# Kernel optimization log

Measured on AMD Instinct MI355X. Metric: run time of the kernel, lower is better.

Reference implementation:

```python
import jax, jax.numpy as jnp
import numpy as np

B, T, S, E, H, D = 4, 1024, 1024, 1024, 16, 64


def _ln(x, g, b, eps=1e-5):
    m = x.mean(-1, keepdims=True)
    v = ((x - m) ** 2).mean(-1, keepdims=True)
    return (x - m) * jax.lax.rsqrt(v + eps) * g + b


def _mha(xq, xkv, mask4, Wq, Wk, Wv, Wo, bo):
    # Wq/Wk/Wv: [H, E, D] (stacked per-head bias-free linears)
    q = jnp.einsum('bte,hed->bhtd', xq, Wq)
    k = jnp.einsum('bse,hed->bhsd', xkv, Wk)
    v = jnp.einsum('bse,hed->bhsd', xkv, Wv)
    # NOTE: original scales by C**-0.5 with C = n_embd, not head_size
    wei = jnp.einsum('bhtd,bhsd->bhts', q, k) * (float(E) ** -0.5)
    wei = jnp.where(mask4 == 0, jnp.float32(-1e9), wei)
    wei = jax.nn.softmax(wei, axis=-1)
    o = jnp.einsum('bhts,bhsd->bhtd', wei, v)  # [B,H,T,D]
    b_, h_, t_, d_ = o.shape
    o = o.transpose(0, 2, 1, 3).reshape(b_, t_, h_ * d_)
    return o @ Wo + bo


def setup_inputs() -> dict:
    key = jax.random.key(0)
    ks = jax.random.split(key, 24)
    sd = 0.02
    inp = {
        'x': jax.random.normal(ks[0], (B, T, E), jnp.float32),
        'x_m': jnp.ones((B, 1, T), jnp.int32),
        'ca': jax.random.normal(ks[1], (B, S, E), jnp.float32),
        'ca_m': jnp.ones((B, 1, S), jnp.int32),
        'Wq_s': jax.random.normal(ks[2], (H, E, D), jnp.float32) * sd,
        'Wk_s': jax.random.normal(ks[3], (H, E, D), jnp.float32) * sd,
        'Wv_s': jax.random.normal(ks[4], (H, E, D), jnp.float32) * sd,
        'Wo_s': jax.random.normal(ks[5], (E, E), jnp.float32) * sd,
        'bo_s': jnp.zeros((E,), jnp.float32),
        'Wq_c': jax.random.normal(ks[6], (H, E, D), jnp.float32) * sd,
        'Wk_c': jax.random.normal(ks[7], (H, E, D), jnp.float32) * sd,
        'Wv_c': jax.random.normal(ks[8], (H, E, D), jnp.float32) * sd,
        'Wo_c': jax.random.normal(ks[9], (E, E), jnp.float32) * sd,
        'bo_c': jnp.zeros((E,), jnp.float32),
        'ln1_g': jnp.ones((E,), jnp.float32), 'ln1_b': jnp.zeros((E,), jnp.float32),
        'ln2_g': jnp.ones((E,), jnp.float32), 'ln2_b': jnp.zeros((E,), jnp.float32),
        'ln3_g': jnp.ones((E,), jnp.float32), 'ln3_b': jnp.zeros((E,), jnp.float32),
        'W1': jax.random.normal(ks[10], (E, 4 * E), jnp.float32) * sd,
        'b1': jnp.zeros((4 * E,), jnp.float32),
        'W2': jax.random.normal(ks[11], (4 * E, E), jnp.float32) * sd,
        'b2': jnp.zeros((E,), jnp.float32),
    }
    return inp


def reference(x, x_m, ca, ca_m, Wq_s, Wk_s, Wv_s, Wo_s, bo_s,
              Wq_c, Wk_c, Wv_c, Wo_c, bo_c,
              ln1_g, ln1_b, ln2_g, ln2_b, ln3_g, ln3_b,
              W1, b1, W2, b2):
    tril = jnp.tril(jnp.ones((T, T), jnp.int32))
    # self-attn mask: x_m [B,1,T] & tril [T,T] -> [B,1,T,T] (broadcast over heads)
    self_mask = x_m[:, :, None, :] * tril          # [B,1,T,T]
    cross_mask = ca_m[:, :, None, :]               # [B,1,1,S]
    x = x + _mha(_ln(x, ln1_g, ln1_b), _ln(x, ln1_g, ln1_b) if False else _ln(x, ln1_g, ln1_b), self_mask, Wq_s, Wk_s, Wv_s, Wo_s, bo_s)
    x = x + _mha(_ln(x, ln2_g, ln2_b), ca, cross_mask, Wq_c, Wk_c, Wv_c, Wo_c, bo_c)
    h = _ln(x, ln3_g, ln3_b)
    x = x + (jax.nn.relu(h @ W1 + b1) @ W2 + b2)
    return x
```

## Files before the change

### kernel.cpp

```cpp
#include <hip/hip_runtime.h>
#include <hip/hip_bf16.h>
#include <cstdint>
#include <cstddef>

typedef __attribute__((ext_vector_type(8))) short  s8v;
typedef __attribute__((ext_vector_type(4))) short  s4v;
typedef __attribute__((ext_vector_type(8))) __bf16 b8v;
typedef __attribute__((ext_vector_type(4))) float  f32x4;
typedef __attribute__((ext_vector_type(4))) unsigned u32x4;

__device__ __forceinline__ short f2bf(float f){
  unsigned u = __builtin_bit_cast(unsigned, f);
  unsigned r = (u + 0x7fffu + ((u >> 16) & 1u)) >> 16;
  return (short)(unsigned short)r;
}

__device__ __forceinline__ f32x4 mfma16(s8v a, s8v b, f32x4 c){
  return __builtin_amdgcn_mfma_f32_16x16x32_bf16(
      __builtin_bit_cast(b8v, a), __builtin_bit_cast(b8v, b), c, 0, 0, 0);
}

__device__ __forceinline__ unsigned cvtpk(float a, float b){
  unsigned w;
  asm("v_cvt_pk_bf16_f32 %0, %1, %2" : "=v"(w) : "v"(a), "v"(b));
  return w;
}

__global__ __launch_bounds__(256)
void ln_k(const float* __restrict__ x, const float* __restrict__ g,
          const float* __restrict__ b, short* __restrict__ out)
{
  const int row = blockIdx.x, tid = threadIdx.x;
  const float4 v = ((const float4*)(x + (size_t)row*1024))[tid];
  float s  = v.x+v.y+v.z+v.w;
  float s2 = v.x*v.x+v.y*v.y+v.z*v.z+v.w*v.w;
  #pragma unroll
  for (int off=32; off; off>>=1){ s += __shfl_down(s, off); s2 += __shfl_down(s2, off); }
  __shared__ float red[8];
  const int wave = tid>>6, lane = tid&63;
  if (lane==0){ red[wave]=s; red[4+wave]=s2; }
  __syncthreads();
  s  = red[0]+red[1]+red[2]+red[3];
  s2 = red[4]+red[5]+red[6]+red[7];
  const float mean = s*(1.f/1024.f);
  const float rstd = rsqrtf(s2*(1.f/1024.f) - mean*mean + 1e-5f);
  const float4 gv = ((const float4*)g)[tid];
  const float4 bv = ((const float4*)b)[tid];
  s4v o;
  o[0] = f2bf((v.x-mean)*rstd*gv.x + bv.x);
  o[1] = f2bf((v.y-mean)*rstd*gv.y + bv.y);
  o[2] = f2bf((v.z-mean)*rstd*gv.z + bv.z);
  o[3] = f2bf((v.w-mean)*rstd*gv.w + bv.w);
  *(s4v*)(out + (size_t)row*1024 + tid*4) = o;
}

__global__ __launch_bounds__(256)
void cast_k(const float* __restrict__ in, short* __restrict__ out)
{
  const int i = blockIdx.x*256 + threadIdx.x;
  const float4 v = ((const float4*)in)[i];
  s4v o; o[0]=f2bf(v.x); o[1]=f2bf(v.y); o[2]=f2bf(v.z); o[3]=f2bf(v.w);
  ((s4v*)out)[i] = o;
}

__global__ __launch_bounds__(256)
void tcast_k(const float* __restrict__ in, short* __restrict__ out, int E2, int D2)
{
  __shared__ float t[32][33];
  const int h  = blockIdx.z;
  const int e0 = blockIdx.x*32, d0 = blockIdx.y*32;
  const int tx = threadIdx.x & 31, ty = threadIdx.x >> 5;
  const float* ip = in + (size_t)h*E2*D2;
  #pragma unroll
  for (int r = ty; r < 32; r += 8)
    t[r][tx] = ip[(size_t)(e0+r)*D2 + d0 + tx];
  __syncthreads();
  short* op = out + (size_t)h*D2*E2;
  #pragma unroll
  for (int r = ty; r < 32; r += 8)
    op[(size_t)(d0+r)*E2 + e0 + tx] = f2bf(t[tx][r]);
}

__global__ __launch_bounds__(256)
void vtrans_k(const short* __restrict__ V, int ldv, short* __restrict__ Vt, int S, int H)
{
  __shared__ short t[32][34];
  const int bh = blockIdx.z;
  const int b = bh / H, h = bh % H;
  const int s0 = blockIdx.x*32, d0 = blockIdx.y*32;
  const int tx = threadIdx.x & 31, ty = threadIdx.x >> 5;
  const short* ip = V + (size_t)b*S*ldv + h*64;
  #pragma unroll
  for (int r = ty; r < 32; r += 8)
    t[r][tx] = ip[(size_t)(s0+r)*ldv + d0 + tx];
  __syncthreads();
  short* op = Vt + ((size_t)bh*64 + d0)*S + s0;
  #pragma unroll
  for (int r = ty; r < 32; r += 8)
    op[(size_t)r*S + tx] = t[tx][r];
}

__global__ __launch_bounds__(256)
void red2_k(const float* __restrict__ pa, const float* __restrict__ pb,
            const float* __restrict__ bias, const float* __restrict__ resid,
            float* __restrict__ out, int N)
{
  const int i = blockIdx.x*256 + threadIdx.x;
  const float4 va = ((const float4*)pa)[i];
  const float4 vb = ((const float4*)pb)[i];
  const float4 vr = ((const float4*)resid)[i];
  const float4 bv = ((const float4*)bias)[i & (N/4 - 1)];
  float4 o;
  o.x = va.x+vb.x+bv.x+vr.x; o.y = va.y+vb.y+bv.y+vr.y;
  o.z = va.z+vb.z+bv.z+vr.z; o.w = va.w+vb.w+bv.w+vr.w;
  ((float4*)out)[i] = o;
}

template<int BN, int BIAS, int RELU, int RESID, int WF32>
__global__ __launch_bounds__(256, 2)
void gemm_bt(const short* __restrict__ A, const short* __restrict__ Bt,
             const float* __restrict__ bias, const float* __restrict__ resid,
             short* __restrict__ Cb, float* __restrict__ Cf,
             int M, int N, int K)
{
  __shared__ short lds[3][128*32 + BN*32];
  const int nwg = gridDim.x * gridDim.y;
  int id = blockIdx.y * gridDim.x + blockIdx.x;
  id = (id & 7) * (nwg >> 3) + (id >> 3);
  const int bx = id % gridDim.x, by = id / gridDim.x;
  const int m0 = by*128, n0 = bx*BN;

  const int tid  = threadIdx.x;
  const int wave = tid>>6, lane = tid&63;
  const int lo = lane&15, hi = lane>>4;
  const int wm = wave>>1, wn = wave&1;

  constexpr int NJ = BN/32;
  constexpr int BC = BN>>6;
  f32x4 acc[4][NJ] = {};
  const int NK = K >> 5;

  auto stage = [&](int buf, int kt){
    const short* Ag = A  + (size_t)m0*K + kt*32;
    const short* Bg = Bt + (size_t)n0*K + kt*32;
    #pragma unroll
    for (int c=0;c<2;c++){
      const int q = (wave*2+c)*64 + lane;
      const int r = q>>2, cc = q&3;
      __builtin_amdgcn_global_load_lds(
        (const __attribute__((address_space(1))) void*)(Ag + (size_t)r*K + cc*8),
        (__attribute__((address_space(3))) void*)(&lds[buf][(wave*2+c)*512]),
        16, 0, 0);
    }
    #pragma unroll
    for (int c=0;c<BC;c++){
      const int q = (wave*BC+c)*64 + lane;
      const int r = q>>2, cc = q&3;
      __builtin_amdgcn_global_load_lds(
        (const __attribute__((address_space(1))) void*)(Bg + (size_t)r*K + cc*8),
        (__attribute__((address_space(3))) void*)(&lds[buf][4096 + (wave*BC+c)*512]),
        16, 0, 0);
    }
  };

  stage(0, 0);
  if (NK > 1) stage(1, 1);

  for (int kt=0; kt<NK; kt++){
    if (kt+1 < NK){
      if constexpr (BN==128) asm volatile("s_waitcnt vmcnt(4)" ::: "memory");
      else                   asm volatile("s_waitcnt vmcnt(3)" ::: "memory");
    } else {
      asm volatile("s_waitcnt vmcnt(0)" ::: "memory");
    }
    __builtin_amdgcn_s_barrier();
    __builtin_amdgcn_sched_barrier(0);
    if (kt+2 < NK) stage((kt+2)%3, kt+2);

    const short* la = &lds[kt%3][0];
    const short* lb = &lds[kt%3][4096];
    s8v af[4], bfr[NJ];
    #pragma unroll
    for (int i=0;i<4;i++)
      af[i] = *(const s8v*)(la + (wm*64 + i*16 + lo)*32 + hi*8);
    #pragma unroll
    for (int j=0;j<NJ;j++)
      bfr[j] = *(const s8v*)(lb + (wn*(BN/2) + j*16 + lo)*32 + hi*8);
    #pragma unroll
    for (int i=0;i<4;i++)
      #pragma unroll
      for (int j=0;j<NJ;j++)
        acc[i][j] = mfma16(af[i], bfr[j], acc[i][j]);
  }

  #pragma unroll
  for (int i=0;i<4;i++){
    const int row = m0 + wm*64 + i*16 + hi*4;
    #pragma unroll
    for (int j=0;j<NJ;j++){
      const int col = n0 + wn*(BN/2) + j*16 + lo;
      const float bv = BIAS ? bias[col] : 0.0f;
      #pragma unroll
      for (int r=0;r<4;r++){
        float v = acc[i][j][r] + bv;
        if (RELU) v = fmaxf(v, 0.0f);
        const size_t idx = (size_t)(row + r)*N + col;
        if (RESID) v += resid[idx];
        if (WF32) Cf[idx] = v; else Cb[idx] = f2bf(v);
      }
    }
  }
}

template<int BIAS, int RELU, int RESID, int WF32>
__global__ __launch_bounds__(512, 1)
void gemm8(const short* __restrict__ A, int lda,
           const short* __restrict__ Bt, int ldb,
           const float* __restrict__ bias, const float* __restrict__ resid,
           short* __restrict__ Cb, float* __restrict__ Cf,
           int M, int N, int K)
{
  __shared__ short lds[3][24576];
  const int nwg = gridDim.x * gridDim.y;
  int id = blockIdx.y * gridDim.x + blockIdx.x;
  id = (id & 7) * (nwg >> 3) + (id >> 3);
  const int bx = id % gridDim.x, by = id / gridDim.x;
  const int m0 = by*256, n0 = bx*128;

  const int tid = threadIdx.x;
  const int lane = tid&63, wave = tid>>6;
  const int lo = lane&15, hi = lane>>4;
  const int wr = wave>>2, wc = wave&3;
  const int x8 = lo&7;

  f32x4 acc[8][2] = {};
  const int NT = K >> 6;

  auto stageA = [&](int buf, int kt, int part){
    const short* Ag = A + (size_t)m0*lda + kt*64;
    #pragma unroll
    for (int j=0;j<2;j++){
      const int q = (part*2+j)*512 + tid;
      const int r = q>>3, c = q&7;
      __builtin_amdgcn_global_load_lds(
        (const __attribute__((address_space(1))) void*)(Ag + (size_t)r*lda + ((c^(r&7))*8)),
        (__attribute__((address_space(3))) void*)(&lds[buf][q*8]), 16, 0, 0);
    }
  };
  auto stageB = [&](int buf, int kt, int part){
    const short* Bg = Bt + (size_t)n0*ldb + kt*64;
    const int q = part*512 + tid;
    const int r = q>>3, c = q&7;
    __builtin_amdgcn_global_load_lds(
      (const __attribute__((address_space(1))) void*)(Bg + (size_t)r*ldb + ((c^(r&7))*8)),
      (__attribute__((address_space(3))) void*)(&lds[buf][16384 + q*8]), 16, 0, 0);
  };

  stageA(0,0,0); stageA(0,0,1); stageB(0,0,0); stageB(0,0,1);
  if (NT>1){ stageA(1,1,0); stageA(1,1,1); stageB(1,1,0); stageB(1,1,1); }
  asm volatile("s_waitcnt vmcnt(6)" ::: "memory");
  __builtin_amdgcn_s_barrier();

  for (int t=0; t<NT; t++){
    const short* la = &lds[t%3][0];
    const short* lb = &lds[t%3][16384];
    const int nb = (t+2)%3;
    const bool pf = (t+2 < NT);
    #pragma unroll
    for (int q=0; q<4; q++){
      const int mh = q>>1, ks = q&1;
      s8v af[4], bf2[2];
      #pragma unroll
      for (int i=0;i<4;i++){
        const int row = wr*128 + (mh*4+i)*16 + lo;
        af[i] = *(const s8v*)(la + row*64 + (((ks*4+hi)^x8)*8));
      }
      #pragma unroll
      for (int j=0;j<2;j++){
        const int row = wc*32 + j*16 + lo;
        bf2[j] = *(const s8v*)(lb + row*64 + (((ks*4+hi)^x8)*8));
      }
      if (pf){
        if      (q==0) stageA(nb, t+2, 0);
        else if (q==1) stageA(nb, t+2, 1);
        else if (q==2) stageB(nb, t+2, 0);
        else           stageB(nb, t+2, 1);
      }
      __builtin_amdgcn_s_barrier();
      asm volatile("s_waitcnt lgkmcnt(0)" ::: "memory");
      __builtin_amdgcn_sched_barrier(0);
      __builtin_amdgcn_s_setprio(1);
      #pragma unroll
      for (int i=0;i<4;i++)
        #pragma unroll
        for (int j=0;j<2;j++)
          acc[mh*4+i][j] = mfma16(af[i], bf2[j], acc[mh*4+i][j]);
      __builtin_amdgcn_s_setprio(0);
      if (q==3 && t+1 < NT){
        if (pf) asm volatile("s_waitcnt vmcnt(6)" ::: "memory");
        else    asm volatile("s_waitcnt vmcnt(0)" ::: "memory");
      }
      __builtin_amdgcn_s_barrier();
    }
  }

  #pragma unroll
  for (int I=0;I<8;I++){
    const int row = m0 + wr*128 + I*16 + hi*4;
    #pragma unroll
    for (int j=0;j<2;j++){
      const int col = n0 + wc*32 + j*16 + lo;
      const float bv = BIAS ? bias[col] : 0.0f;
      #pragma unroll
      for (int r=0;r<4;r++){
        float v = acc[I][j][r] + bv;
        if (RELU) v = fmaxf(v, 0.0f);
        const size_t idx = (size_t)(row + r)*N + col;
        if (RESID) v += resid[idx];
        if (WF32) Cf[idx] = v; else Cb[idx] = f2bf(v);
      }
    }
  }
}

template<int CAUSAL>
__global__ __launch_bounds__(256, 4)
void attn_k(const short* __restrict__ Q, int ldq,
            const short* __restrict__ K, int ldk,
            const short* __restrict__ Vt, int ldvt,
            const int* __restrict__ msk,
            short* __restrict__ O, int ldo,
            int H, int Tq, int Sk)
{
  __shared__ short kls[2][4096];
  __shared__ short vls[2][4096];
  const int bh = blockIdx.x;
  const int b = bh / H, h = bh % H;
  const int tid = threadIdx.x;
  const int wave = tid>>6, lane = tid&63;
  const int lo = lane&15, hi = lane>>4;
  const int t0 = blockIdx.y*64 + wave*16;

  const short* Qb  = Q + (size_t)(b*Tq)*ldq + h*64;
  const short* Kb  = K + (size_t)(b*Sk)*ldk + h*64;
  const short* Vtb = Vt + (size_t)bh*64*ldvt;
  const int*   mb  = msk + (size_t)b*Sk;

  const short* qp = Qb + (size_t)(t0+lo)*ldq + hi*8;
  const s8v qa0 = *(const s8v*)(qp);
  const s8v qa1 = *(const s8v*)(qp + 32);

  float mrow = -INFINITY, lrow = 0.f;
  f32x4 oacc[4] = {};
  const int trow = t0 + lo;
  const int nblk = CAUSAL ? (blockIdx.y + 1) : (Sk>>6);
  const float sc2 = 0.03125f * 1.44269504088896f;
  const int x8 = lo & 7;

  auto stage = [&](int buf, int it){
    const int s0 = it*64;
    #pragma unroll
    for (int rd=0; rd<2; rd++){
      const int q = rd*256 + tid;
      const int r = q>>3, c = q&7;
      const int cs = (c ^ (r&7))*8;
      __builtin_amdgcn_global_load_lds(
        (const __attribute__((address_space(1))) void*)(Kb + (size_t)(s0+r)*ldk + cs),
        (__attribute__((address_space(3))) void*)(&kls[buf][(rd*256 + wave*64)*8]),
        16, 0, 0);
      __builtin_amdgcn_global_load_lds(
        (const __attribute__((address_space(1))) void*)(Vtb + (size_t)r*ldvt + s0 + cs),
        (__attribute__((address_space(3))) void*)(&vls[buf][(rd*256 + wave*64)*8]),
        16, 0, 0);
    }
  };

  stage(0, 0);
  int cur = 0;
  for (int it=0; it<nblk; it++){
    __syncthreads();
    if (it+1 < nblk) stage(cur^1, it+1);
    const int s0 = it*64;

    int ka[4][4];
    #pragma unroll
    for (int g=0; g<4; g++){
      const int4 kv = ((const int4*)mb)[(s0>>2) + g*4 + hi];
      ka[g][0]=kv.x; ka[g][1]=kv.y; ka[g][2]=kv.z; ka[g][3]=kv.w;
    }

    const short* kl = kls[cur];
    s8v kf[4][2];
    #pragma unroll
    for (int g=0; g<4; g++){
      const int rb = (g*16 + lo)*64;
      kf[g][0] = *(const s8v*)(kl + rb + ((hi     ^ x8)*8));
      kf[g][1] = *(const s8v*)(kl + rb + (((4+hi) ^ x8)*8));
    }

    f32x4 sg[4] = {};
    __builtin_amdgcn_s_setprio(1);
    #pragma unroll
    for (int g=0; g<4; g++){
      sg[g] = mfma16(kf[g][0], qa0, sg[g]);
      sg[g] = mfma16(kf[g][1], qa1, sg[g]);
    }
    __builtin_amdgcn_s_setprio(0);

    const bool lastblk = CAUSAL && (it == nblk-1);
    float p[4][4];
    #pragma unroll
    for (int g=0; g<4; g++)
      #pragma unroll
      for (int r=0; r<4; r++){
        const int sidx = s0 + g*16 + 4*hi + r;
        const bool ok = ka[g][r] && (!lastblk || sidx <= trow);
        p[g][r] = ok ? sg[g][r]*sc2 : -1.5e9f;
      }

    float bmax;
    {
      float m0_ = fmaxf(fmaxf(p[0][0],p[0][1]), fmaxf(p[0][2],p[0][3]));
      float m1_ = fmaxf(fmaxf(p[1][0],p[1][1]), fmaxf(p[1][2],p[1][3]));
      float m2_ = fmaxf(fmaxf(p[2][0],p[2][1]), fmaxf(p[2][2],p[2][3]));
      float m3_ = fmaxf(fmaxf(p[3][0],p[3][1]), fmaxf(p[3][2],p[3][3]));
      bmax = fmaxf(fmaxf(m0_,m1_), fmaxf(m2_,m3_));
    }
    bmax = fmaxf(bmax, __shfl_xor(bmax, 16));
    bmax = fmaxf(bmax, __shfl_xor(bmax, 32));

    const float mn  = fmaxf(mrow, bmax);
    const float fac = exp2f(mrow - mn);
    mrow = mn;
    #pragma unroll
    for (int g=0; g<4; g++)
      #pragma unroll
      for (int r=0; r<4; r++)
        p[g][r] = exp2f(p[g][r] - mn);

    float bsum;
    {
      float s0_ = (p[0][0]+p[0][1]) + (p[0][2]+p[0][3]);
      float s1_ = (p[1][0]+p[1][1]) + (p[1][2]+p[1][3]);
      float s2_ = (p[2][0]+p[2][1]) + (p[2][2]+p[2][3]);
      float s3_ = (p[3][0]+p[3][1]) + (p[3][2]+p[3][3]);
      bsum = (s0_+s1_) + (s2_+s3_);
    }
    bsum += __shfl_xor(bsum, 16);
    bsum += __shfl_xor(bsum, 32);
    lrow = lrow*fac + bsum;
    #pragma unroll
    for (int f=0; f<4; f++)
      #pragma unroll
      for (int r=0; r<4; r++)
        oacc[f][r] *= fac;

    u32x4 pw0, pw1;
    pw0[0] = cvtpk(p[0][0], p[0][1]);
    pw0[1] = cvtpk(p[0][2], p[0][3]);
    pw0[2] = cvtpk(p[1][0], p[1][1]);
    pw0[3] = cvtpk(p[1][2], p[1][3]);
    pw1[0] = cvtpk(p[2][0], p[2][1]);
    pw1[1] = cvtpk(p[2][2], p[2][3]);
    pw1[2] = cvtpk(p[3][0], p[3][1]);
    pw1[3] = cvtpk(p[3][2], p[3][3]);
    const s8v pb0 = __builtin_bit_cast(s8v, pw0);
    const s8v pb1 = __builtin_bit_cast(s8v, pw1);

    const short* vl = vls[cur];
    __builtin_amdgcn_s_setprio(1);
    #pragma unroll
    for (int f=0; f<4; f++){
      const int rb = (f*16 + lo)*64;
      const int h2 = hi>>1, o2 = (hi&1)*4;
      const s4v a0 = *(const s4v*)(vl + rb + (((h2  ) ^ x8)*8) + o2);
      const s4v a1 = *(const s4v*)(vl + rb + (((2+h2) ^ x8)*8) + o2);
      const s4v a2 = *(const s4v*)(vl + rb + (((4+h2) ^ x8)*8) + o2);
      const s4v a3 = *(const s4v*)(vl + rb + (((6+h2) ^ x8)*8) + o2);
      const s8v av0 = __builtin_shufflevector(a0, a1, 0,1,2,3,4,5,6,7);
      const s8v av1 = __builtin_shufflevector(a2, a3, 0,1,2,3,4,5,6,7);
      oacc[f] = mfma16(av0, pb0, oacc[f]);
      oacc[f] = mfma16(av1, pb1, oacc[f]);
    }
    __builtin_amdgcn_s_setprio(0);
    cur ^= 1;
  }

  const float inv = 1.0f / lrow;
  short* Ob = O + (size_t)(b*Tq)*ldo + h*64 + (size_t)(t0+lo)*ldo + 4*hi;
  #pragma unroll
  for (int f=0; f<4; f++){
    s4v o;
    #pragma unroll
    for (int r=0; r<4; r++) o[r] = f2bf(oacc[f][r]*inv);
    *(s4v*)(Ob + f*16) = o;
  }
}

extern "C" void kernel_launch(void* const* d_in, const int* in_sizes, int n_in,
                              void* d_out, int out_size, void* d_ws, size_t ws_size,
                              hipStream_t stream)
{
  (void)in_sizes; (void)n_in; (void)out_size; (void)ws_size;
  const float* x    = (const float*)d_in[0];
  const int*   xm   = (const int*)  d_in[1];
  const float* ca   = (const float*)d_in[2];
  const int*   cam  = (const int*)  d_in[3];
  const float* Wq_s = (const float*)d_in[4];
  const float* Wk_s = (const float*)d_in[5];
  const float* Wv_s = (const float*)d_in[6];
  const float* Wo_s = (const float*)d_in[7];
  const float* bo_s = (const float*)d_in[8];
  const float* Wq_c = (const float*)d_in[9];
  const float* Wk_c = (const float*)d_in[10];
  const float* Wv_c = (const float*)d_in[11];
  const float* Wo_c = (const float*)d_in[12];
  const float* bo_c = (const float*)d_in[13];
  const float* ln1g = (const float*)d_in[14];
  const float* ln1b = (const float*)d_in[15];
  const float* ln2g = (const float*)d_in[16];
  const float* ln2b = (const float*)d_in[17];
  const float* ln3g = (const float*)d_in[18];
  const float* ln3b = (const float*)d_in[19];
  const float* W1   = (const float*)d_in[20];
  const float* b1   = (const float*)d_in[21];
  const float* W2   = (const float*)d_in[22];
  const float* b2   = (const float*)d_in[23];
  float* out = (float*)d_out;

  char* ws = (char*)d_ws;
  size_t off = 0;
  auto alloc = [&](size_t bytes)->void*{
    void* p = ws + off; off += (bytes + 255) & ~(size_t)255; return p; };

  short* w_qkv_s = (short*)alloc((size_t)3072*1024*2);
  short* w_o_s   = (short*)alloc((size_t)1024*1024*2);
  short* w_q_c   = (short*)alloc((size_t)1024*1024*2);
  short* w_kv_c  = (short*)alloc((size_t)2048*1024*2);
  short* w_o_c   = (short*)alloc((size_t)1024*1024*2);
  short* w_1     = (short*)alloc((size_t)4096*1024*2);
  short* w_2     = (short*)alloc((size_t)1024*4096*2);
  short* xn      = (short*)alloc((size_t)4096*1024*2);
  short* cab     = (short*)alloc((size_t)4096*1024*2);
  short* qkv     = (short*)alloc((size_t)4096*3072*2);
  short* attno   = (short*)alloc((size_t)4096*1024*2);
  float* xres    = (float*)alloc((size_t)4096*1024*4);
  short* hffn    = (short*)alloc((size_t)4096*4096*2);
  float* pA      = (float*)alloc((size_t)4096*1024*4);
  float* pB      = (float*)alloc((size_t)4096*1024*4);
  short* kvbuf   = qkv + (size_t)4096*1024;
  short* vt_s    = hffn;
  short* vt_c    = hffn + (size_t)4*1024*1024;

  tcast_k<<<dim3(32,  2,16),256,0,stream>>>(Wq_s, w_qkv_s,           1024,   64);
  tcast_k<<<dim3(32,  2,16),256,0,stream>>>(Wk_s, w_qkv_s+1024*1024, 1024,   64);
  tcast_k<<<dim3(32,  2,16),256,0,stream>>>(Wv_s, w_qkv_s+2048*1024, 1024,   64);
  tcast_k<<<dim3(32, 32, 1),256,0,stream>>>(Wo_s, w_o_s,             1024, 1024);
  tcast_k<<<dim3(32,  2,16),256,0,stream>>>(Wq_c, w_q_c,             1024,   64);
  tcast_k<<<dim3(32,  2,16),256,0,stream>>>(Wk_c, w_kv_c,            1024,   64);
  tcast_k<<<dim3(32,  2,16),256,0,stream>>>(Wv_c, w_kv_c+1024*1024,  1024,   64);
  tcast_k<<<dim3(32, 32, 1),256,0,stream>>>(Wo_c, w_o_c,             1024, 1024);
  tcast_k<<<dim3(32,128, 1),256,0,stream>>>(W1,   w_1,               1024, 4096);
  tcast_k<<<dim3(128,32, 1),256,0,stream>>>(W2,   w_2,               4096, 1024);
  cast_k<<<4096,256,0,stream>>>(ca, cab);

  ln_k<<<4096,256,0,stream>>>(x, ln1g, ln1b, xn);
  gemm8<0,0,0,0><<<dim3(24,16),512,0,stream>>>(xn, 1024, w_qkv_s, 1024,
                                               nullptr, nullptr, qkv, nullptr,
                                               4096, 3072, 1024);
  vtrans_k<<<dim3(32,2,64),256,0,stream>>>(qkv+2048, 3072, vt_s, 1024, 16);
  attn_k<1><<<dim3(64,16),256,0,stream>>>(qkv, 3072, qkv+1024, 3072, vt_s, 1024,
                                          xm, attno, 1024, 16, 1024, 1024);
  gemm_bt<64,1,0,1,1><<<dim3(16,32),256,0,stream>>>(attno, w_o_s, bo_s, x,
                                                    nullptr, xres, 4096, 1024, 1024);

  ln_k<<<4096,256,0,stream>>>(xres, ln2g, ln2b, xn);
  gemm_bt<64,0,0,0,0><<<dim3(16,32),256,0,stream>>>(xn, w_q_c, nullptr, nullptr,
                                                    qkv, nullptr, 4096, 1024, 1024);
  gemm8<0,0,0,0><<<dim3(16,16),512,0,stream>>>(cab, 1024, w_kv_c, 1024,
                                               nullptr, nullptr, kvbuf, nullptr,
                                               4096, 2048, 1024);
  vtrans_k<<<dim3(32,2,64),256,0,stream>>>(kvbuf+1024, 2048, vt_c, 1024, 16);
  attn_k<0><<<dim3(64,16),256,0,stream>>>(qkv, 1024, kvbuf, 2048, vt_c, 1024,
                                          cam, attno, 1024, 16, 1024, 1024);
  gemm_bt<64,1,0,1,1><<<dim3(16,32),256,0,stream>>>(attno, w_o_c, bo_c, xres,
                                                    nullptr, xres, 4096, 1024, 1024);

  ln_k<<<4096,256,0,stream>>>(xres, ln3g, ln3b, xn);
  gemm8<1,1,0,0><<<dim3(32,16),512,0,stream>>>(xn, 1024, w_1, 1024,
                                               b1, nullptr, hffn, nullptr,
                                               4096, 4096, 1024);
  gemm8<0,0,0,1><<<dim3(8,16),512,0,stream>>>(hffn,      4096, w_2,      4096,
                                              nullptr, nullptr, nullptr, pA,
                                              4096, 1024, 2048);
  gemm8<0,0,0,1><<<dim3(8,16),512,0,stream>>>(hffn+2048, 4096, w_2+2048, 4096,
                                              nullptr, nullptr, nullptr, pB,
                                              4096, 1024, 2048);
  red2_k<<<4096,256,0,stream>>>(pA, pB, b2, xres, out, 1024);
}
```

Before: 434.3 us.

## Use 256x256 GEMM tiles with double buffering and 4-way split-K FFN down-projection

Replaces the 256x128 triple-buffered GEMM with a 256x256-tile double-buffered kernel, which doubles the MFMA work per LDS load and halves the number of workgroups. The FFN down-projection now uses a 4-way split-K along grid z, writing bf16 partials that a new reduction kernel sums together with the bias and residual. The larger tile raises data reuse but lowers occupancy and grid parallelism, and the bf16 partials trade some precision for less memory traffic.

Result: faster. 378.9 us (-12.7%).

```diff
diff --git a/kernel.cpp b/kernel.cpp
--- a/kernel.cpp
+++ b/kernel.cpp
@@ -13,6 +13,9 @@
   unsigned u = __builtin_bit_cast(unsigned, f);
   unsigned r = (u + 0x7fffu + ((u >> 16) & 1u)) >> 16;
   return (short)(unsigned short)r;
+}
+__device__ __forceinline__ float bf2f(short s){
+  return __builtin_bit_cast(float, ((unsigned)(unsigned short)s) << 16);
 }
 
 __device__ __forceinline__ f32x4 mfma16(s8v a, s8v b, f32x4 c){
@@ -101,18 +104,18 @@
 }
 
 __global__ __launch_bounds__(256)
-void red2_k(const float* __restrict__ pa, const float* __restrict__ pb,
-            const float* __restrict__ bias, const float* __restrict__ resid,
-            float* __restrict__ out, int N)
+void red4_k(const short* __restrict__ p, const float* __restrict__ bias,
+            const float* __restrict__ resid, float* __restrict__ out)
 {
   const int i = blockIdx.x*256 + threadIdx.x;
-  const float4 va = ((const float4*)pa)[i];
-  const float4 vb = ((const float4*)pb)[i];
-  const float4 vr = ((const float4*)resid)[i];
-  const float4 bv = ((const float4*)bias)[i & (N/4 - 1)];
-  float4 o;
-  o.x = va.x+vb.x+bv.x+vr.x; o.y = va.y+vb.y+bv.y+vr.y;
-  o.z = va.z+vb.z+bv.z+vr.z; o.w = va.w+vb.w+bv.w+vr.w;
+  float4 o = ((const float4*)resid)[i];
+  const float4 bv = ((const float4*)bias)[i & 255];
+  o.x += bv.x; o.y += bv.y; o.z += bv.z; o.w += bv.w;
+  #pragma unroll
+  for (int z=0; z<4; z++){
+    const s4v v = ((const s4v*)(p + (size_t)z*4194304))[i];
+    o.x += bf2f(v[0]); o.y += bf2f(v[1]); o.z += bf2f(v[2]); o.w += bf2f(v[3]);
+  }
   ((float4*)out)[i] = o;
 }
 
@@ -214,38 +217,37 @@
 
 template<int BIAS, int RELU, int RESID, int WF32>
 __global__ __launch_bounds__(512, 1)
-void gemm8(const short* __restrict__ A, int lda,
-           const short* __restrict__ Bt, int ldb,
-           const float* __restrict__ bias, const float* __restrict__ resid,
-           short* __restrict__ Cb, float* __restrict__ Cf,
-           int M, int N, int K)
-{
-  __shared__ short lds[3][24576];
+void gemm256(const short* __restrict__ A, int lda,
+             const short* __restrict__ Bt, int ldb,
+             const float* __restrict__ bias, const float* __restrict__ resid,
+             short* __restrict__ Cb, float* __restrict__ Cf,
+             int M, int N, int K)
+{
+  __shared__ short lds[2][32768];
   const int nwg = gridDim.x * gridDim.y;
   int id = blockIdx.y * gridDim.x + blockIdx.x;
   id = (id & 7) * (nwg >> 3) + (id >> 3);
   const int bx = id % gridDim.x, by = id / gridDim.x;
-  const int m0 = by*256, n0 = bx*128;
+  const int m0 = by*256, n0 = bx*256;
+  A  += (size_t)blockIdx.z * K;
+  Bt += (size_t)blockIdx.z * K;
+  const size_t cofs = (size_t)blockIdx.z * M * N;
 
   const int tid = threadIdx.x;
   const int lane = tid&63, wave = tid>>6;
   const int lo = lane&15, hi = lane>>4;
   const int wr = wave>>2, wc = wave&3;
-  const int x8 = lo&7;
-
-  f32x4 acc[8][2] = {};
+
+  f32x4 acc[8][4] = {};
   const int NT = K >> 6;
 
   auto stageA = [&](int buf, int kt, int part){
     const short* Ag = A + (size_t)m0*lda + kt*64;
-    #pragma unroll
-    for (int j=0;j<2;j++){
-      const int q = (part*2+j)*512 + tid;
-      const int r = q>>3, c = q&7;
-      __builtin_amdgcn_global_load_lds(
-        (const __attribute__((address_space(1))) void*)(Ag + (size_t)r*lda + ((c^(r&7))*8)),
-        (__attribute__((address_space(3))) void*)(&lds[buf][q*8]), 16, 0, 0);
-    }
+    const int q = part*512 + tid;
+    const int r = q>>3, c = q&7;
+    __builtin_amdgcn_global_load_lds(
+      (const __attribute__((address_space(1))) void*)(Ag + (size_t)r*lda + ((c^(r&7))*8)),
+      (__attribute__((address_space(3))) void*)(&lds[buf][q*8]), 16, 0, 0);
   };
   auto stageB = [&](int buf, int kt, int part){
     const short* Bg = Bt + (size_t)n0*ldb + kt*64;
@@ -256,66 +258,59 @@
       (__attribute__((address_space(3))) void*)(&lds[buf][16384 + q*8]), 16, 0, 0);
   };
 
-  stageA(0,0,0); stageA(0,0,1); stageB(0,0,0); stageB(0,0,1);
-  if (NT>1){ stageA(1,1,0); stageA(1,1,1); stageB(1,1,0); stageB(1,1,1); }
-  asm volatile("s_waitcnt vmcnt(6)" ::: "memory");
-  __builtin_amdgcn_s_barrier();
+  #pragma unroll
+  for (int p=0;p<4;p++){ stageA(0,0,p); stageB(0,0,p); }
+  __syncthreads();
 
   for (int t=0; t<NT; t++){
-    const short* la = &lds[t%3][0];
-    const short* lb = &lds[t%3][16384];
-    const int nb = (t+2)%3;
-    const bool pf = (t+2 < NT);
-    #pragma unroll
-    for (int q=0; q<4; q++){
-      const int mh = q>>1, ks = q&1;
-      s8v af[4], bf2[2];
-      #pragma unroll
-      for (int i=0;i<4;i++){
-        const int row = wr*128 + (mh*4+i)*16 + lo;
-        af[i] = *(const s8v*)(la + row*64 + (((ks*4+hi)^x8)*8));
+    const int cur = t&1;
+    const short* la = &lds[cur][0];
+    const short* lb = &lds[cur][16384];
+    const bool pf = (t+1 < NT);
+    #pragma unroll
+    for (int ks=0; ks<2; ks++){
+      s8v bf[4];
+      #pragma unroll
+      for (int j=0;j<4;j++){
+        const int r = wc*64 + j*16 + lo;
+        bf[j] = *(const s8v*)(lb + r*64 + (((ks*4+hi)^(r&7))*8));
       }
       #pragma unroll
-      for (int j=0;j<2;j++){
-        const int row = wc*32 + j*16 + lo;
-        bf2[j] = *(const s8v*)(lb + row*64 + (((ks*4+hi)^x8)*8));
+      for (int mh=0; mh<2; mh++){
+        s8v af[4];
+        #pragma unroll
+        for (int i=0;i<4;i++){
+          const int r = wr*128 + mh*64 + i*16 + lo;
+          af[i] = *(const s8v*)(la + r*64 + (((ks*4+hi)^(r&7))*8));
+        }
+        if (pf && ks==0){
+          stageA(cur^1, t+1, mh*2);   stageB(cur^1, t+1, mh*2);
+          stageA(cur^1, t+1, mh*2+1); stageB(cur^1, t+1, mh*2+1);
+        }
+        __builtin_amdgcn_s_setprio(1);
+        #pragma unroll
+        for (int i=0;i<4;i++)
+          #pragma unroll
+          for (int j=0;j<4;j++)
+            acc[mh*4+i][j] = mfma16(af[i], bf[j], acc[mh*4+i][j]);
+        __builtin_amdgcn_s_setprio(0);
       }
-      if (pf){
-        if      (q==0) stageA(nb, t+2, 0);
-        else if (q==1) stageA(nb, t+2, 1);
-        else if (q==2) stageB(nb, t+2, 0);
-        else           stageB(nb, t+2, 1);
-      }
-      __builtin_amdgcn_s_barrier();
-      asm volatile("s_waitcnt lgkmcnt(0)" ::: "memory");
-      __builtin_amdgcn_sched_barrier(0);
-      __builtin_amdgcn_s_setprio(1);
-      #pragma unroll
-      for (int i=0;i<4;i++)
-        #pragma unroll
-        for (int j=0;j<2;j++)
-          acc[mh*4+i][j] = mfma16(af[i], bf2[j], acc[mh*4+i][j]);
-      __builtin_amdgcn_s_setprio(0);
-      if (q==3 && t+1 < NT){
-        if (pf) asm volatile("s_waitcnt vmcnt(6)" ::: "memory");
-        else    asm volatile("s_waitcnt vmcnt(0)" ::: "memory");
-      }
-      __builtin_amdgcn_s_barrier();
-    }
+    }
+    __syncthreads();
   }
 
   #pragma unroll
   for (int I=0;I<8;I++){
     const int row = m0 + wr*128 + I*16 + hi*4;
     #pragma unroll
-    for (int j=0;j<2;j++){
-      const int col = n0 + wc*32 + j*16 + lo;
+    for (int j=0;j<4;j++){
+      const int col = n0 + wc*64 + j*16 + lo;
       const float bv = BIAS ? bias[col] : 0.0f;
       #pragma unroll
       for (int r=0;r<4;r++){
         float v = acc[I][j][r] + bv;
         if (RELU) v = fmaxf(v, 0.0f);
-        const size_t idx = (size_t)(row + r)*N + col;
+        const size_t idx = cofs + (size_t)(row + r)*N + col;
         if (RESID) v += resid[idx];
         if (WF32) Cf[idx] = v; else Cb[idx] = f2bf(v);
       }
@@ -548,9 +543,11 @@
   short* hffn    = (short*)alloc((size_t)4096*4096*2);
   float* pA      = (float*)alloc((size_t)4096*1024*4);
   float* pB      = (float*)alloc((size_t)4096*1024*4);
+  short* pP      = (short*)pA;
   short* kvbuf   = qkv + (size_t)4096*1024;
   short* vt_s    = hffn;
   short* vt_c    = hffn + (size_t)4*1024*1024;
+  (void)pB;
 
   tcast_k<<<dim3(32,  2,16),256,0,stream>>>(Wq_s, w_qkv_s,           1024,   64);
   tcast_k<<<dim3(32,  2,16),256,0,stream>>>(Wk_s, w_qkv_s+1024*1024, 1024,   64);
@@ -565,9 +562,9 @@
   cast_k<<<4096,256,0,stream>>>(ca, cab);
 
   ln_k<<<4096,256,0,stream>>>(x, ln1g, ln1b, xn);
-  gemm8<0,0,0,0><<<dim3(24,16),512,0,stream>>>(xn, 1024, w_qkv_s, 1024,
-                                               nullptr, nullptr, qkv, nullptr,
-                                               4096, 3072, 1024);
+  gemm256<0,0,0,0><<<dim3(12,16),512,0,stream>>>(xn, 1024, w_qkv_s, 1024,
+                                                 nullptr, nullptr, qkv, nullptr,
+                                                 4096, 3072, 1024);
   vtrans_k<<<dim3(32,2,64),256,0,stream>>>(qkv+2048, 3072, vt_s, 1024, 16);
   attn_k<1><<<dim3(64,16),256,0,stream>>>(qkv, 3072, qkv+1024, 3072, vt_s, 1024,
                                           xm, attno, 1024, 16, 1024, 1024);
@@ -577,9 +574,9 @@
   ln_k<<<4096,256,0,stream>>>(xres, ln2g, ln2b, xn);
   gemm_bt<64,0,0,0,0><<<dim3(16,32),256,0,stream>>>(xn, w_q_c, nullptr, nullptr,
                                                     qkv, nullptr, 4096, 1024, 1024);
-  gemm8<0,0,0,0><<<dim3(16,16),512,0,stream>>>(cab, 1024, w_kv_c, 1024,
-                                               nullptr, nullptr, kvbuf, nullptr,
-                                               4096, 2048, 1024);
+  gemm256<0,0,0,0><<<dim3(8,16),512,0,stream>>>(cab, 1024, w_kv_c, 1024,
+                                                nullptr, nullptr, kvbuf, nullptr,
+                                                4096, 2048, 1024);
   vtrans_k<<<dim3(32,2,64),256,0,stream>>>(kvbuf+1024, 2048, vt_c, 1024, 16);
   attn_k<0><<<dim3(64,16),256,0,stream>>>(qkv, 1024, kvbuf, 2048, vt_c, 1024,
                                           cam, attno, 1024, 16, 1024, 1024);
@@ -587,14 +584,11 @@
                                                     nullptr, xres, 4096, 1024, 1024);
 
   ln_k<<<4096,256,0,stream>>>(xres, ln3g, ln3b, xn);
-  gemm8<1,1,0,0><<<dim3(32,16),512,0,stream>>>(xn, 1024, w_1, 1024,
-                                               b1, nullptr, hffn, nullptr,
-                                               4096, 4096, 1024);
-  gemm8<0,0,0,1><<<dim3(8,16),512,0,stream>>>(hffn,      4096, w_2,      4096,
-                                              nullptr, nullptr, nullptr, pA,
-                                              4096, 1024, 2048);
-  gemm8<0,0,0,1><<<dim3(8,16),512,0,stream>>>(hffn+2048, 4096, w_2+2048, 4096,
-                                              nullptr, nullptr, nullptr, pB,
-                                              4096, 1024, 2048);
-  red2_k<<<4096,256,0,stream>>>(pA, pB, b2, xres, out, 1024);
-}
+  gemm256<1,1,0,0><<<dim3(16,16),512,0,stream>>>(xn, 1024, w_1, 1024,
+                                                 b1, nullptr, hffn, nullptr,
+                                                 4096, 4096, 1024);
+  gemm256<0,0,0,0><<<dim3(4,16,4),512,0,stream>>>(hffn, 4096, w_2, 4096,
+                                                  nullptr, nullptr, pP, nullptr,
+                                                  4096, 1024, 1024);
+  red4_k<<<4096,256,0,stream>>>(pP, b2, xres, out);
+}
```
